# Kernel tuning notes

Hardware: AMD Instinct MI355X
Metric: run time of the kernel (lower is better)

The kernel has to match this reference:

```python
import jax, jax.numpy as jnp
import numpy as np

B, N, D = 4, 2048, 768
OUT = 768

def setup_inputs() -> dict:
    key = jax.random.key(0)
    k1, k2 = jax.random.split(key)
    x = jax.random.normal(k1, (B, N, D), dtype=jnp.float32)
    kernel = jax.random.normal(k2, (3, D, OUT), dtype=jnp.float32) * 0.02
    return {"x": x, "kernel": kernel}

def reference(x, kernel):
    # Single-head attention with shared QKV kernel stack [3, D, OUT]
    q = jnp.einsum('bnd,do->bno', x, kernel[0])
    k = jnp.einsum('bnd,do->bno', x, kernel[1])
    v = jnp.einsum('bnd,do->bno', x, kernel[2])
    # NOTE: original divides by 64**0.5 == 8 regardless of dims (faithful)
    scores = jnp.einsum('bqo,bko->bqk', q, k) / 8.0
    attn = jax.nn.softmax(scores, axis=-1)
    return jnp.einsum('bqk,bko->bqo', attn, v)
```

## Files before the change

### kernel.cpp

```cpp
#include <hip/hip_runtime.h>
#include <hip/hip_bf16.h>

constexpr int B_ = 4, N_ = 2048, D_ = 768, OUT_ = 768;
constexpr int M_ = B_ * N_;

typedef __attribute__((ext_vector_type(8))) short short8;
typedef __attribute__((ext_vector_type(4))) float floatx4;

__device__ __forceinline__ unsigned short f2bfu(float f) {
    union { __hip_bfloat16 b; unsigned short u; } cv;
    cv.b = __float2bfloat16(f);
    return cv.u;
}

#define GLOAD_LDS16(g, l)                                                     \
    __builtin_amdgcn_global_load_lds(                                         \
        (const __attribute__((address_space(1))) void*)(g),                   \
        (__attribute__((address_space(3))) void*)(l), 16, 0, 0)

#define MFMA_BF16 __builtin_amdgcn_mfma_f32_16x16x32_bf16
#define SBAR __builtin_amdgcn_s_barrier
#define SCHED0 __builtin_amdgcn_sched_barrier

template <int MFR, int NT>
__device__ __forceinline__ void gemm_tb(
    const __hip_bfloat16* __restrict__ aG, int lda,
    const __hip_bfloat16* __restrict__ bG, int ldb,
    unsigned short* LDS, floatx4 (&acc)[MFR][4]) {
    constexpr int BSLOT = (MFR == 4) ? 8192 : 4096;
    constexpr int BUFS = 4096 + BSLOT;
    constexpr int LOADS = (MFR == 4) ? 3 : 2;
    const int tid = threadIdx.x;
    const int wave = tid >> 6, lane = tid & 63;
    const int lr = lane & 15, kq = lane >> 4;
    const int wm = (MFR == 4) ? (wave >> 2) * 64 : (wave >> 1) * 32;
    const int wn = (MFR == 4) ? (wave & 3) * 64 : (wave & 1) * 64;

    const int p0 = tid >> 3, g0 = (tid & 7) ^ (p0 & 7);
    const __hip_bfloat16* pa =
        aG + (size_t)(2 * p0 + (g0 >> 2)) * lda + (g0 & 3) * 8;
    const __hip_bfloat16* pb0 =
        bG + (size_t)(2 * p0 + (g0 >> 2)) * ldb + (g0 & 3) * 8;
    const __hip_bfloat16* pb1 = bG;
    if constexpr (MFR == 4) {
        const int u = 512 + tid, p1 = u >> 3, g1 = (u & 7) ^ (p1 & 7);
        pb1 = bG + (size_t)(2 * p1 + (g1 >> 2)) * ldb + (g1 & 3) * 8;
    }

    int oa[MFR], ob[4];
#pragma unroll
    for (int mi = 0; mi < MFR; ++mi) {
        const int r = wm + mi * 16 + lr, p = r >> 1;
        const int g = ((r & 1) << 2) | kq;
        oa[mi] = p * 64 + ((g ^ (p & 7)) * 8);
    }
#pragma unroll
    for (int ni = 0; ni < 4; ++ni) {
        const int r = wn + ni * 16 + lr, p = r >> 1;
        const int g = ((r & 1) << 2) | kq;
        ob[ni] = p * 64 + ((g ^ (p & 7)) * 8);
    }

    auto STAGE = [&](int tt, int buf) {
        unsigned short* d = LDS + buf * BUFS + wave * 512;
        GLOAD_LDS16(pa + tt * 32, d);
        GLOAD_LDS16(pb0 + tt * 32, d + 4096);
        if constexpr (MFR == 4) GLOAD_LDS16(pb1 + tt * 32, d + 8192);
    };

    STAGE(0, 0);
    STAGE(1, 1);
    asm volatile("s_waitcnt vmcnt(%0)" ::"i"(LOADS) : "memory");
    SBAR();
    SCHED0(0);

    int bR = 0, bS = 2;
    for (int t = 0; t < NT; ++t) {
        const unsigned short* Ab = LDS + bR * BUFS;
        const unsigned short* Bb = Ab + 4096;
        short8 af[MFR], bf[4];
#pragma unroll
        for (int mi = 0; mi < MFR; ++mi)
            af[mi] = *(const short8*)(Ab + oa[mi]);
#pragma unroll
        for (int ni = 0; ni < 4; ++ni)
            bf[ni] = *(const short8*)(Bb + ob[ni]);
        if (t + 2 < NT) STAGE(t + 2, bS);
#pragma unroll
        for (int mi = 0; mi < MFR; ++mi)
#pragma unroll
            for (int ni = 0; ni < 4; ++ni)
                acc[mi][ni] = MFMA_BF16(af[mi], bf[ni], acc[mi][ni], 0, 0, 0);
        if (t + 2 < NT)
            asm volatile("s_waitcnt vmcnt(%0)" ::"i"(LOADS) : "memory");
        else if (t + 1 < NT)
            asm volatile("s_waitcnt vmcnt(0)" ::: "memory");
        if (t + 1 < NT) {
            SBAR();
            SCHED0(0);
        }
        bR = (bR == 2) ? 0 : bR + 1;
        bS = (bS == 2) ? 0 : bS + 1;
    }
}

__global__ __launch_bounds__(256)
void prep(const float* __restrict__ x, const float* __restrict__ w,
          __hip_bfloat16* __restrict__ xb, __hip_bfloat16* __restrict__ wt,
          float* __restrict__ l) {
    __shared__ float t[32][33];
    const int tid = threadIdx.x;
    if (blockIdx.x < 3072) {
        const size_t i = (size_t)blockIdx.x * 2048 + (size_t)tid * 8;
        float4 a = *(const float4*)(x + i);
        float4 b = *(const float4*)(x + i + 4);
        *(ushort4*)((unsigned short*)xb + i) =
            make_ushort4(f2bfu(a.x), f2bfu(a.y), f2bfu(a.z), f2bfu(a.w));
        *(ushort4*)((unsigned short*)xb + i + 4) =
            make_ushort4(f2bfu(b.x), f2bfu(b.y), f2bfu(b.z), f2bfu(b.w));
    } else if (blockIdx.x < 4800) {
        const int bid = blockIdx.x - 3072;
        const int s = bid / 576, rem = bid % 576;
        const int d0 = (rem / 24) * 32, o0 = (rem % 24) * 32;
        const int tx = tid & 31, ty = tid >> 5;
        const float* ws = w + (size_t)s * D_ * OUT_;
        __hip_bfloat16* wts = wt + (size_t)s * OUT_ * D_;
#pragma unroll
        for (int i = 0; i < 4; ++i)
            t[ty + 8 * i][tx] = ws[(size_t)(d0 + ty + 8 * i) * OUT_ + o0 + tx];
        __syncthreads();
#pragma unroll
        for (int i = 0; i < 4; ++i)
            wts[(size_t)(o0 + ty + 8 * i) * D_ + d0 + tx] =
                __float2bfloat16(t[tx][ty + 8 * i]);
    } else {
        float4* l4 = (float4*)l;
#pragma unroll
        for (int i = 0; i < 8; ++i) l4[i * 256 + tid] = make_float4(0, 0, 0, 0);
    }
}

__global__ __launch_bounds__(512, 4)
void qkv_mfma(const __hip_bfloat16* __restrict__ xb,
              const __hip_bfloat16* __restrict__ wt,
              __hip_bfloat16* __restrict__ q, __hip_bfloat16* __restrict__ k,
              __hip_bfloat16* __restrict__ vt) {
    __shared__ __align__(16) unsigned short LDS[36864];
    const int s = blockIdx.z;
    const int m0 = blockIdx.x * 128, n0 = blockIdx.y * 256;
    floatx4 acc[4][4] = {};
    gemm_tb<4, 24>(xb + (size_t)m0 * D_, D_,
                   wt + (size_t)s * OUT_ * D_ + (size_t)n0 * D_, D_, LDS, acc);

    const int tid = threadIdx.x, wave = tid >> 6, lane = tid & 63;
    const int lrow = lane & 15, kq = lane >> 4;
    const int wm = (wave >> 2) * 64, wn = (wave & 3) * 64;
    unsigned short* E = LDS;

    if (s < 2) {
        __syncthreads();
#pragma unroll
        for (int mi = 0; mi < 4; ++mi)
#pragma unroll
            for (int ni = 0; ni < 4; ++ni) {
                const int n = wn + ni * 16 + lrow;
#pragma unroll
                for (int r = 0; r < 4; ++r)
                    E[(wm + mi * 16 + kq * 4 + r) * 264 + n] =
                        f2bfu(acc[mi][ni][r]);
            }
        __syncthreads();
        unsigned short* outp = (unsigned short*)(s == 0 ? q : k);
#pragma unroll
        for (int i = 0; i < 8; ++i) {
            const int u = i * 512 + tid, row = u >> 5, c = u & 31;
            *(short8*)(outp + (size_t)(m0 + row) * OUT_ + n0 + c * 8) =
                *(const short8*)(E + row * 264 + c * 8);
        }
    } else {
        __syncthreads();
#pragma unroll
        for (int mi = 0; mi < 4; ++mi)
#pragma unroll
            for (int ni = 0; ni < 4; ++ni) {
                const int n = wn + ni * 16 + lrow;
#pragma unroll
                for (int r = 0; r < 4; ++r)
                    E[n * 136 + wm + mi * 16 + kq * 4 + r] =
                        f2bfu(acc[mi][ni][r]);
            }
        __syncthreads();
        const int b = m0 >> 11, j0 = m0 & 2047;
#pragma unroll
        for (int i = 0; i < 8; ++i) {
            const int u = i * 512 + tid, nr = u >> 4, c = u & 15;
            *(short8*)((unsigned short*)vt + ((size_t)b * OUT_ + n0 + nr) * N_ +
                       j0 + c * 8) = *(const short8*)(E + nr * 136 + c * 8);
        }
    }
}

__global__ __launch_bounds__(512, 4)
void scores_mfma(const __hip_bfloat16* __restrict__ q,
                 const __hip_bfloat16* __restrict__ k,
                 __hip_bfloat16* __restrict__ pt, float* __restrict__ l) {
    __shared__ __align__(16) unsigned short LDS[36864];
    const int b = blockIdx.z;
    const int m0 = blockIdx.x * 128, n0 = blockIdx.y * 256;
    floatx4 acc[4][4] = {};
    gemm_tb<4, 24>(q + (size_t)b * N_ * OUT_ + (size_t)m0 * OUT_, OUT_,
                   k + (size_t)b * N_ * OUT_ + (size_t)n0 * OUT_, OUT_, LDS,
                   acc);

    const int tid = threadIdx.x, wave = tid >> 6, lane = tid & 63;
    const int lrow = lane & 15, kq = lane >> 4;
    const int wm = (wave >> 2) * 64, wn = (wave & 3) * 64;

    float rs[4][4];
#pragma unroll
    for (int mi = 0; mi < 4; ++mi)
#pragma unroll
        for (int r = 0; r < 4; ++r) rs[mi][r] = 0.0f;
#pragma unroll
    for (int mi = 0; mi < 4; ++mi)
#pragma unroll
        for (int ni = 0; ni < 4; ++ni)
#pragma unroll
            for (int r = 0; r < 4; ++r) {
                const float e = __expf(acc[mi][ni][r] * 0.125f - 8.0f);
                acc[mi][ni][r] = e;
                rs[mi][r] += e;
            }
#pragma unroll
    for (int mi = 0; mi < 4; ++mi)
#pragma unroll
        for (int r = 0; r < 4; ++r) {
            float v = rs[mi][r];
            v += __shfl_xor(v, 1, 64);
            v += __shfl_xor(v, 2, 64);
            v += __shfl_xor(v, 4, 64);
            v += __shfl_xor(v, 8, 64);
            if (lrow == 0)
                atomicAdd(&l[(size_t)b * N_ + m0 + wm + mi * 16 + kq * 4 + r],
                          v);
        }

    unsigned short* E = LDS;
    unsigned short* pb = (unsigned short*)pt + (size_t)b * N_ * N_;
    __syncthreads();
#pragma unroll
    for (int mi = 0; mi < 4; ++mi)
#pragma unroll
        for (int ni = 0; ni < 4; ++ni) {
            const int n = wn + ni * 16 + lrow;
#pragma unroll
            for (int r = 0; r < 4; ++r)
                E[(wm + mi * 16 + kq * 4 + r) * 258 + n] =
                    f2bfu(acc[mi][ni][r]);
        }
    __syncthreads();
#pragma unroll
    for (int i = 0; i < 8; ++i) {
        const int u = i * 512 + tid, row = u >> 5, c = u & 31;
        *(short8*)(pb + (size_t)(m0 + row) * N_ + n0 + c * 8) =
            *(const short8*)(E + row * 258 + c * 8);
    }
}

__global__ __launch_bounds__(512, 4)
void pv_mfma(const __hip_bfloat16* __restrict__ pt,
             const __hip_bfloat16* __restrict__ vt,
             const float* __restrict__ l, float* __restrict__ out) {
    __shared__ __align__(16) unsigned short LDS[24576];
    const int b = blockIdx.z;
    const int m0 = blockIdx.x * 128, n0 = blockIdx.y * 128;
    floatx4 acc[2][4] = {};
    gemm_tb<2, 64>(pt + (size_t)b * N_ * N_ + (size_t)m0 * N_, N_,
                   vt + (size_t)b * OUT_ * N_ + (size_t)n0 * N_, N_, LDS, acc);

    const int tid = threadIdx.x, wave = tid >> 6, lane = tid & 63;
    const int lrow = lane & 15, kq = lane >> 4;
    const int wm = (wave >> 1) * 32, wn = (wave & 1) * 64;
    const float* lb = l + (size_t)b * N_ + m0 + wm;
#pragma unroll
    for (int mi = 0; mi < 2; ++mi)
#pragma unroll
        for (int r = 0; r < 4; ++r) {
            const float inv = 1.0f / lb[mi * 16 + kq * 4 + r];
            float* o = out +
                       ((size_t)b * N_ + m0 + wm + mi * 16 + kq * 4 + r) *
                           OUT_ +
                       n0 + wn;
#pragma unroll
            for (int ni = 0; ni < 4; ++ni)
                o[ni * 16 + lrow] = acc[mi][ni][r] * inv;
        }
}

extern "C" void kernel_launch(void* const* d_in, const int* in_sizes, int n_in,
                              void* d_out, int out_size, void* d_ws,
                              size_t ws_size, hipStream_t stream) {
    const float* x = (const float*)d_in[0];
    const float* w = (const float*)d_in[1];
    float* out = (float*)d_out;

    __hip_bfloat16* q  = (__hip_bfloat16*)d_ws;
    __hip_bfloat16* k  = q + (size_t)M_ * OUT_;
    __hip_bfloat16* vt = k + (size_t)M_ * OUT_;
    __hip_bfloat16* xb = vt + (size_t)M_ * OUT_;
    __hip_bfloat16* wt = xb + (size_t)M_ * D_;
    float* l = (float*)(wt + (size_t)3 * OUT_ * D_);
    __hip_bfloat16* pt = (__hip_bfloat16*)(l + M_);

    prep<<<dim3(4801), dim3(256), 0, stream>>>(x, w, xb, wt, l);
    qkv_mfma<<<dim3(64, 3, 3), dim3(512), 0, stream>>>(xb, wt, q, k, vt);
    scores_mfma<<<dim3(16, 8, 4), dim3(512), 0, stream>>>(q, k, pt, l);
    pv_mfma<<<dim3(16, 6, 4), dim3(512), 0, stream>>>(pt, vt, l, out);
}
```

Baseline: 189.7 us.

## Retile PV GEMM to 64x256 blocks with 4-wave workgroups

Adds a new GEMM routine that gives each 256-thread block a 64-row by 256-column output tile, with every wave covering all 64 rows and its own 64 columns. The PV kernel switches from 128x128 tiles with 8 waves to this shape, so each P row tile is read by fewer blocks and the V columns are split into three 256-wide slices. The generic gemm_tb is also reworked to always stage two B loads, which increases B traffic for the MFR==2 path. The risk is fewer waves per block, which can hurt latency hiding, and a grid of 384 blocks.

```diff
diff --git a/kernel.cpp b/kernel.cpp
--- a/kernel.cpp
+++ b/kernel.cpp
@@ -39,12 +39,11 @@
     const int p0 = tid >> 3, g0 = (tid & 7) ^ (p0 & 7);
     const __hip_bfloat16* pa =
         aG + (size_t)(2 * p0 + (g0 >> 2)) * lda + (g0 & 3) * 8;
-    const __hip_bfloat16* pb0 =
-        bG + (size_t)(2 * p0 + (g0 >> 2)) * ldb + (g0 & 3) * 8;
-    const __hip_bfloat16* pb1 = bG;
-    if constexpr (MFR == 4) {
-        const int u = 512 + tid, p1 = u >> 3, g1 = (u & 7) ^ (p1 & 7);
-        pb1 = bG + (size_t)(2 * p1 + (g1 >> 2)) * ldb + (g1 & 3) * 8;
+    const __hip_bfloat16* pb[2];
+#pragma unroll
+    for (int j = 0; j < 2; ++j) {
+        const int u = j * 512 + tid, p = u >> 3, g = (u & 7) ^ (p & 7);
+        pb[j] = bG + (size_t)(2 * p + (g >> 2)) * ldb + (g & 3) * 8;
     }
 
     int oa[MFR], ob[4];
@@ -58,14 +57,15 @@
     for (int ni = 0; ni < 4; ++ni) {
         const int r = wn + ni * 16 + lr, p = r >> 1;
         const int g = ((r & 1) << 2) | kq;
-        ob[ni] = p * 64 + ((g ^ (p & 7)) * 8);
+        ob[ni] = 4096 + p * 64 + ((g ^ (p & 7)) * 8);
     }
 
     auto STAGE = [&](int tt, int buf) {
         unsigned short* d = LDS + buf * BUFS + wave * 512;
         GLOAD_LDS16(pa + tt * 32, d);
-        GLOAD_LDS16(pb0 + tt * 32, d + 4096);
-        if constexpr (MFR == 4) GLOAD_LDS16(pb1 + tt * 32, d + 8192);
+#pragma unroll
+        for (int j = 0; j < 2; ++j)
+            GLOAD_LDS16(pb[j] + tt * 32, d + 4096 + j * 4096);
     };
 
     STAGE(0, 0);
@@ -77,14 +77,13 @@
     int bR = 0, bS = 2;
     for (int t = 0; t < NT; ++t) {
         const unsigned short* Ab = LDS + bR * BUFS;
-        const unsigned short* Bb = Ab + 4096;
         short8 af[MFR], bf[4];
 #pragma unroll
         for (int mi = 0; mi < MFR; ++mi)
             af[mi] = *(const short8*)(Ab + oa[mi]);
 #pragma unroll
         for (int ni = 0; ni < 4; ++ni)
-            bf[ni] = *(const short8*)(Bb + ob[ni]);
+            bf[ni] = *(const short8*)(Ab + ob[ni]);
         if (t + 2 < NT) STAGE(t + 2, bS);
 #pragma unroll
         for (int mi = 0; mi < MFR; ++mi)
@@ -93,6 +92,79 @@
                 acc[mi][ni] = MFMA_BF16(af[mi], bf[ni], acc[mi][ni], 0, 0, 0);
         if (t + 2 < NT)
             asm volatile("s_waitcnt vmcnt(%0)" ::"i"(LOADS) : "memory");
+        else if (t + 1 < NT)
+            asm volatile("s_waitcnt vmcnt(0)" ::: "memory");
+        if (t + 1 < NT) {
+            SBAR();
+            SCHED0(0);
+        }
+        bR = (bR == 2) ? 0 : bR + 1;
+        bS = (bS == 2) ? 0 : bS + 1;
+    }
+}
+
+template <int NT>
+__device__ __forceinline__ void gemm_n256(
+    const __hip_bfloat16* __restrict__ aG, int lda,
+    const __hip_bfloat16* __restrict__ bG, int ldb,
+    unsigned short* LDS, floatx4 (&acc)[4][4]) {
+    constexpr int BUFS = 10240;
+    const int tid = threadIdx.x;
+    const int wave = tid >> 6, lane = tid & 63;
+    const int lr = lane & 15, kq = lane >> 4;
+    const int wn = wave * 64;
+
+    const int p0 = tid >> 3, g0 = (tid & 7) ^ (p0 & 7);
+    const __hip_bfloat16* pa =
+        aG + (size_t)(2 * p0 + (g0 >> 2)) * lda + (g0 & 3) * 8;
+    const __hip_bfloat16* pb[4];
+#pragma unroll
+    for (int j = 0; j < 4; ++j) {
+        const int u = j * 256 + tid, p = u >> 3, g = (u & 7) ^ (p & 7);
+        pb[j] = bG + (size_t)(2 * p + (g >> 2)) * ldb + (g & 3) * 8;
+    }
+
+    int oa[4], ob[4];
+#pragma unroll
+    for (int i = 0; i < 4; ++i) {
+        const int ra = i * 16 + lr, pA = ra >> 1;
+        const int gA = ((ra & 1) << 2) | kq;
+        oa[i] = pA * 64 + ((gA ^ (pA & 7)) * 8);
+        const int rb = wn + i * 16 + lr, pB = rb >> 1;
+        const int gB = ((rb & 1) << 2) | kq;
+        ob[i] = 2048 + pB * 64 + ((gB ^ (pB & 7)) * 8);
+    }
+
+    auto STAGE = [&](int tt, int buf) {
+        unsigned short* d = LDS + buf * BUFS + wave * 512;
+        GLOAD_LDS16(pa + tt * 32, d);
+#pragma unroll
+        for (int j = 0; j < 4; ++j)
+            GLOAD_LDS16(pb[j] + tt * 32, d + 2048 + j * 2048);
+    };
+
+    STAGE(0, 0);
+    STAGE(1, 1);
+    asm volatile("s_waitcnt vmcnt(5)" ::: "memory");
+    SBAR();
+    SCHED0(0);
+
+    int bR = 0, bS = 2;
+    for (int t = 0; t < NT; ++t) {
+        const unsigned short* Ab = LDS + bR * BUFS;
+        short8 af[4], bf[4];
+#pragma unroll
+        for (int mi = 0; mi < 4; ++mi) af[mi] = *(const short8*)(Ab + oa[mi]);
+#pragma unroll
+        for (int ni = 0; ni < 4; ++ni) bf[ni] = *(const short8*)(Ab + ob[ni]);
+        if (t + 2 < NT) STAGE(t + 2, bS);
+#pragma unroll
+        for (int mi = 0; mi < 4; ++mi)
+#pragma unroll
+            for (int ni = 0; ni < 4; ++ni)
+                acc[mi][ni] = MFMA_BF16(af[mi], bf[ni], acc[mi][ni], 0, 0, 0);
+        if (t + 2 < NT)
+            asm volatile("s_waitcnt vmcnt(5)" ::: "memory");
         else if (t + 1 < NT)
             asm volatile("s_waitcnt vmcnt(0)" ::: "memory");
         if (t + 1 < NT) {
@@ -267,30 +339,28 @@
     }
 }
 
-__global__ __launch_bounds__(512, 4)
+__global__ __launch_bounds__(256, 2)
 void pv_mfma(const __hip_bfloat16* __restrict__ pt,
              const __hip_bfloat16* __restrict__ vt,
              const float* __restrict__ l, float* __restrict__ out) {
-    __shared__ __align__(16) unsigned short LDS[24576];
+    __shared__ __align__(16) unsigned short LDS[30720];
     const int b = blockIdx.z;
-    const int m0 = blockIdx.x * 128, n0 = blockIdx.y * 128;
-    floatx4 acc[2][4] = {};
-    gemm_tb<2, 64>(pt + (size_t)b * N_ * N_ + (size_t)m0 * N_, N_,
-                   vt + (size_t)b * OUT_ * N_ + (size_t)n0 * N_, N_, LDS, acc);
+    const int m0 = blockIdx.x * 64, n0 = blockIdx.y * 256;
+    floatx4 acc[4][4] = {};
+    gemm_n256<64>(pt + (size_t)b * N_ * N_ + (size_t)m0 * N_, N_,
+                  vt + (size_t)b * OUT_ * N_ + (size_t)n0 * N_, N_, LDS, acc);
 
     const int tid = threadIdx.x, wave = tid >> 6, lane = tid & 63;
     const int lrow = lane & 15, kq = lane >> 4;
-    const int wm = (wave >> 1) * 32, wn = (wave & 1) * 64;
-    const float* lb = l + (size_t)b * N_ + m0 + wm;
-#pragma unroll
-    for (int mi = 0; mi < 2; ++mi)
+    const int wn = wave * 64;
+    const float* lb = l + (size_t)b * N_ + m0;
+#pragma unroll
+    for (int mi = 0; mi < 4; ++mi)
 #pragma unroll
         for (int r = 0; r < 4; ++r) {
-            const float inv = 1.0f / lb[mi * 16 + kq * 4 + r];
-            float* o = out +
-                       ((size_t)b * N_ + m0 + wm + mi * 16 + kq * 4 + r) *
-                           OUT_ +
-                       n0 + wn;
+            const int row = mi * 16 + kq * 4 + r;
+            const float inv = 1.0f / lb[row];
+            float* o = out + ((size_t)b * N_ + m0 + row) * OUT_ + n0 + wn;
 #pragma unroll
             for (int ni = 0; ni < 4; ++ni)
                 o[ni * 16 + lrow] = acc[mi][ni][r] * inv;
@@ -315,5 +385,5 @@
     prep<<<dim3(4801), dim3(256), 0, stream>>>(x, w, xb, wt, l);
     qkv_mfma<<<dim3(64, 3, 3), dim3(512), 0, stream>>>(xb, wt, q, k, vt);
     scores_mfma<<<dim3(16, 8, 4), dim3(512), 0, stream>>>(q, k, pt, l);
-    pv_mfma<<<dim3(16, 6, 4), dim3(512), 0, stream>>>(pt, vt, l, out);
-}
+    pv_mfma<<<dim3(32, 3, 4), dim3(256), 0, stream>>>(pt, vt, l, out);
+}
```

Result: slower. 203.4 us (+7.2%).
